# Optimization experiments

Measured on AMD Instinct MI355X. Metric: run time of the kernel, lower is better.

## Reference

```python
import jax, jax.numpy as jnp
import numpy as np

B, T, N, D, E = 16, 12, 512, 128, 32  # batch, time, nodes, model_dim, node_emb_dim


def setup_inputs() -> dict:
    key = jax.random.key(0)
    ks = jax.random.split(key, 7)
    return {
        "value": jax.random.normal(ks[0], (B, T, N, D), dtype=jnp.float32),
        "emb": jax.random.normal(ks[1], (T, N, E), dtype=jnp.float32),
        "attn_mask": jax.random.randint(ks[2], (B, N, N), 0, 2, dtype=jnp.int32),
        "W_qk": jax.random.normal(ks[3], (E, D), dtype=jnp.float32) * (1.0 / np.sqrt(E)),
        "b_qk": jax.random.normal(ks[4], (D,), dtype=jnp.float32) * 0.02,
        "W_v": jax.random.normal(ks[5], (D, D), dtype=jnp.float32) * (1.0 / np.sqrt(D)),
        "b_v": jax.random.normal(ks[6], (D,), dtype=jnp.float32) * 0.02,
    }


def reference(value, emb, attn_mask, W_qk, b_qk, W_v, b_v):
    # qk projection shared between query and key: [T, N, D]
    qk = emb @ W_qk + b_qk
    # query: softmax over feature dim D
    q = jax.nn.softmax(qk, axis=-1)                      # [T, N, D]
    # key: transpose then softmax over node dim N
    k = jax.nn.softmax(jnp.swapaxes(qk, -1, -2), axis=-1)  # [T, D, N]
    # value projection (note: out_proj in __init__ is unused in forward)
    v = value @ W_v + b_v                                # [B, T, N, D]
    # batch-independent base attention score, then broadcast over batch
    score = jnp.einsum('tnd,tdm->tnm', q, k)             # [T, N, N]
    score = jnp.broadcast_to(score[None], (value.shape[0],) + score.shape)  # [B, T, N, N]
    # masked fill: mask [B, N, N] -> [B, 1, N, N]
    score = jnp.where(attn_mask[:, None] == 0, jnp.float32(-1e9), score)
    out = jnp.einsum('btnm,btmd->btnd', score, v)         # [B, T, N, D]
    return out
```

## Files before the change

### kernel.cpp

```cpp
#include <hip/hip_runtime.h>

#define B_ 16
#define T_ 12
#define N_ 512
#define D_ 128
#define E_ 32

typedef __attribute__((ext_vector_type(8))) unsigned short u16x8;
typedef __attribute__((ext_vector_type(8))) __bf16 bf16x8;
typedef __attribute__((ext_vector_type(4))) float f32x4;

static __device__ __forceinline__ unsigned short f2bf(float f) {
    unsigned u = __float_as_uint(f);
    unsigned r = (u + 0x7fffu + ((u >> 16) & 1u)) >> 16;
    return (unsigned short)r;
}

static __device__ __forceinline__ void gld16(const void* src, void* dst) {
    __builtin_amdgcn_global_load_lds(
        (const __attribute__((address_space(1))) unsigned*)src,
        (__attribute__((address_space(3))) unsigned*)dst, 16, 0, 0);
}

__global__ __launch_bounds__(256) void k1(const float* __restrict__ emb,
                                          const float* __restrict__ Wqk,
                                          const float* __restrict__ bqk,
                                          unsigned short* __restrict__ qb,
                                          unsigned short* __restrict__ kN,
                                          const float* __restrict__ Wv,
                                          unsigned short* __restrict__ WvT,
                                          const int* __restrict__ mask,
                                          unsigned* __restrict__ mb) {
    __shared__ __align__(16) char LE[256 * 128];
    __shared__ float red[2][4][8];
    int hwid = blockIdx.x;
    int bid = (hwid & 7) * 144 + (hwid >> 3);
    int tid = threadIdx.x;

    if (bid < 192) {
        int t = bid >> 4;
        int d0 = (bid & 15) * 8;
        int dc = tid & 7, ni = tid >> 3;
        int wave = tid >> 6, lane = tid & 63;
        int l3 = lane >> 3, l7 = lane & 7;
        float wqv[E_];
#pragma unroll
        for (int e = 0; e < E_; ++e) wqv[e] = Wqk[e * D_ + d0 + dc];
        float bq = bqk[d0 + dc];
        const char* eb = (const char*)(emb + (size_t)t * N_ * E_);

        float vals[16];
#pragma unroll
        for (int pass = 0; pass < 2; ++pass) {
#pragma unroll
            for (int it = 0; it < 8; ++it) {
                int rl = it * 32 + wave * 8 + l3;
                int rg = pass * 256 + rl;
                gld16(eb + (size_t)rg * 128 + ((l7 * 16) ^ ((rg & 7) << 4)),
                      LE + (it * 32 + wave * 8) * 128 + lane * 16);
            }
            __syncthreads();
#pragma unroll
            for (int jj = 0; jj < 8; ++jj) {
                int n = pass * 256 + ni + 32 * jj;
                int nl = ni + 32 * jj;
                float a = bq;
#pragma unroll
                for (int s = 0; s < 8; ++s) {
                    f32x4 ev = *(const f32x4*)(LE + nl * 128 +
                                               ((s * 16) ^ ((n & 7) << 4)));
                    a = fmaf(ev[0], wqv[s * 4 + 0], a);
                    a = fmaf(ev[1], wqv[s * 4 + 1], a);
                    a = fmaf(ev[2], wqv[s * 4 + 2], a);
                    a = fmaf(ev[3], wqv[s * 4 + 3], a);
                }
                vals[pass * 8 + jj] = a;
            }
            __syncthreads();
        }

        float mx = -1e30f;
#pragma unroll
        for (int j = 0; j < 16; ++j) mx = fmaxf(mx, vals[j]);
#pragma unroll
        for (int s = 8; s < 64; s <<= 1) mx = fmaxf(mx, __shfl_xor(mx, s));
        int wv = tid >> 6;
        if ((tid & 63) < 8) red[0][wv][dc] = mx;
        __syncthreads();
        mx = fmaxf(fmaxf(red[0][0][dc], red[0][1][dc]),
                   fmaxf(red[0][2][dc], red[0][3][dc]));
        float sum = 0.f;
#pragma unroll
        for (int j = 0; j < 16; ++j) {
            vals[j] = __expf(vals[j] - mx);
            sum += vals[j];
        }
#pragma unroll
        for (int s = 8; s < 64; s <<= 1) sum += __shfl_xor(sum, s);
        if ((tid & 63) < 8) red[1][wv][dc] = sum;
        __syncthreads();
        sum = red[1][0][dc] + red[1][1][dc] + red[1][2][dc] + red[1][3][dc];
        float inv = 1.f / sum;
        unsigned short* op = kN + (size_t)t * N_ * D_ + d0 + dc;
#pragma unroll
        for (int j = 0; j < 16; ++j)
            op[(size_t)(ni + 32 * j) * D_] = f2bf(vals[j] * inv);
        return;
    }

    if (bid < 576) {
        int bid2 = bid - 192;
        int w = tid >> 6, l = tid & 63;
        float wq0[E_], wq1[E_];
#pragma unroll
        for (int e = 0; e < E_; ++e) {
            wq0[e] = Wqk[e * D_ + l];
            wq1[e] = Wqk[e * D_ + l + 64];
        }
        float b0 = bqk[l], b1 = bqk[l + 64];
        for (int rr = 0; rr < 4; ++rr) {
            int tn = bid2 * 16 + w * 4 + rr;
            const float* ep = emb + (size_t)tn * E_;
            float a0 = b0, a1 = b1;
#pragma unroll
            for (int e = 0; e < E_; ++e) {
                float ev = ep[e];
                a0 = fmaf(ev, wq0[e], a0);
                a1 = fmaf(ev, wq1[e], a1);
            }
            float mx = fmaxf(a0, a1);
#pragma unroll
            for (int s = 32; s > 0; s >>= 1) mx = fmaxf(mx, __shfl_xor(mx, s));
            float e0 = __expf(a0 - mx), e1 = __expf(a1 - mx);
            float sum = e0 + e1;
#pragma unroll
            for (int s = 32; s > 0; s >>= 1) sum += __shfl_xor(sum, s);
            float inv = 1.f / sum;
            qb[(size_t)tn * D_ + l] = f2bf(e0 * inv);
            qb[(size_t)tn * D_ + l + 64] = f2bf(e1 * inv);
        }
        return;
    }

    if (bid < 1088) {
        int o = (bid - 576) * 256 + tid;
        const int* mp = mask + (size_t)o * 32;
        unsigned bits = 0;
#pragma unroll
        for (int j = 0; j < 32; j += 4) {
            int4 m4 = *(const int4*)&mp[j];
            bits |= (m4.x ? 1u : 0u) << j;
            bits |= (m4.y ? 1u : 0u) << (j + 1);
            bits |= (m4.z ? 1u : 0u) << (j + 2);
            bits |= (m4.w ? 1u : 0u) << (j + 3);
        }
        mb[o] = bits;
        return;
    }

    {
        int i = (bid - 1088) * 256 + tid;
        int d = i >> 7, k = i & 127;
        WvT[d * 128 + k] = f2bf(Wv[k * 128 + d]);
    }
}

__global__ __launch_bounds__(256, 2) void kF(const unsigned short* __restrict__ qb,
                                             const unsigned short* __restrict__ kN,
                                             unsigned short* __restrict__ sc,
                                             const float* __restrict__ value,
                                             const unsigned short* __restrict__ WvT,
                                             const float* __restrict__ bv,
                                             unsigned short* __restrict__ vT) {
    __shared__ __align__(16) char LA[2][128 * 128];
    __shared__ __align__(16) char LB[2][128 * 128];
    int hwid = blockIdx.x;
    int bid = (hwid & 7) * 120 + (hwid >> 3);
    int tid = threadIdx.x;
    int wave = tid >> 6, lane = tid & 63;
    int q = lane >> 4, lr = lane & 15;
    int rbase = (wave & 1) * 64, cbase = (wave >> 1) * 64;
    int l3 = lane >> 3, l7 = lane & 7;

    f32x4 acc[4][4];
#pragma unroll
    for (int i = 0; i < 4; ++i)
#pragma unroll
        for (int j = 0; j < 4; ++j) acc[i][j] = (f32x4){0.f, 0.f, 0.f, 0.f};

#define STAGE_T(gbase, lb, c)                                                   \
    _Pragma("unroll") for (int it_ = 0; it_ < 4; ++it_) {                       \
        int row_ = it_ * 32 + wave * 8 + l3;                                    \
        gld16((gbase) + (size_t)row_ * 256 + (c) * 128 +                        \
                  ((l7 * 16) ^ ((row_ & 7) << 4)),                              \
              (lb) + (it_ * 32 + wave * 8) * 128 + lane * 16);                  \
    }

#define MFMA_CHUNK(c)                                                           \
    _Pragma("unroll") for (int ksl_ = 0; ksl_ < 2; ++ksl_) {                    \
        bf16x8 a_[4], b_[4];                                                    \
        _Pragma("unroll") for (int i_ = 0; i_ < 4; ++i_) {                      \
            int r_ = rbase + 16 * i_ + lr;                                      \
            a_[i_] = *(const bf16x8*)(LA[c] + r_ * 128 +                        \
                                      ((ksl_ * 64 + q * 16) ^ ((r_ & 7) << 4)));\
        }                                                                       \
        _Pragma("unroll") for (int j_ = 0; j_ < 4; ++j_) {                      \
            int r_ = cbase + 16 * j_ + lr;                                      \
            b_[j_] = *(const bf16x8*)(LB[c] + r_ * 128 +                        \
                                      ((ksl_ * 64 + q * 16) ^ ((r_ & 7) << 4)));\
        }                                                                       \
        _Pragma("unroll") for (int i_ = 0; i_ < 4; ++i_)                        \
            _Pragma("unroll") for (int j_ = 0; j_ < 4; ++j_)                    \
                acc[i_][j_] = __builtin_amdgcn_mfma_f32_16x16x32_bf16(          \
                    a_[i_], b_[j_], acc[i_][j_], 0, 0, 0);                      \
    }

    if (bid < 192) {
        int mt = bid & 3, nt = (bid >> 2) & 3, t = bid >> 4;
        int n0 = nt * 128, m0 = mt * 128;
        const char* qp = (const char*)(qb + (size_t)t * N_ * D_ + (size_t)n0 * D_);
        const char* kp = (const char*)(kN + (size_t)t * N_ * D_ + (size_t)m0 * D_);
        STAGE_T(qp, LA[0], 0)
        STAGE_T(kp, LB[0], 0)
        STAGE_T(qp, LA[1], 1)
        STAGE_T(kp, LB[1], 1)
        asm volatile("s_waitcnt vmcnt(8)" ::: "memory");
        __builtin_amdgcn_sched_barrier(0);
        __builtin_amdgcn_s_barrier();
        __builtin_amdgcn_sched_barrier(0);
        MFMA_CHUNK(0)
        asm volatile("s_waitcnt vmcnt(0)" ::: "memory");
        __builtin_amdgcn_sched_barrier(0);
        __builtin_amdgcn_s_barrier();
        __builtin_amdgcn_sched_barrier(0);
        MFMA_CHUNK(1)

        unsigned short* sp = sc + (size_t)t * N_ * N_;
#pragma unroll
        for (int i = 0; i < 4; ++i)
#pragma unroll
            for (int j = 0; j < 4; ++j) {
                int row0 = n0 + rbase + 16 * i + q * 4;
                int col = m0 + cbase + 16 * j + lr;
#pragma unroll
                for (int e = 0; e < 4; ++e)
                    sp[(size_t)(row0 + e) * N_ + col] = f2bf(acc[i][j][e]);
            }
        return;
    }

    {
        int idx = bid - 192;
        int mt = idx & 3, bt = idx >> 2;
        int m0 = mt * 128;
        const float* vp = value + ((size_t)bt * N_ + m0) * D_;
        const char* wp = (const char*)WvT;
        int g = tid >> 4, c16 = tid & 15;

        float4 v0[8], v1[8];
#pragma unroll
        for (int jj = 0; jj < 8; ++jj)
            v0[jj] = *(const float4*)(vp + (size_t)(g * 8 + jj) * D_ + c16 * 4);
        __builtin_amdgcn_sched_barrier(0);
        STAGE_T(wp, LA[0], 0)
        __builtin_amdgcn_sched_barrier(0);
#pragma unroll
        for (int jj = 0; jj < 8; ++jj)
            v1[jj] = *(const float4*)(vp + (size_t)(g * 8 + jj) * D_ + 64 + c16 * 4);
        __builtin_amdgcn_sched_barrier(0);
        STAGE_T(wp, LA[1], 1)
        __builtin_amdgcn_sched_barrier(0);

#pragma unroll
        for (int jj = 0; jj < 8; ++jj) {
            int row = g * 8 + jj;
            ushort4 o;
            o.x = f2bf(v0[jj].x); o.y = f2bf(v0[jj].y);
            o.z = f2bf(v0[jj].z); o.w = f2bf(v0[jj].w);
            *(ushort4*)(LB[0] + row * 128 + ((c16 * 8) ^ ((row & 7) << 4))) = o;
        }
        asm volatile("s_waitcnt vmcnt(12) lgkmcnt(0)" ::: "memory");
        __builtin_amdgcn_sched_barrier(0);
        __builtin_amdgcn_s_barrier();
        __builtin_amdgcn_sched_barrier(0);
        MFMA_CHUNK(0)
#pragma unroll
        for (int jj = 0; jj < 8; ++jj) {
            int row = g * 8 + jj;
            ushort4 o;
            o.x = f2bf(v1[jj].x); o.y = f2bf(v1[jj].y);
            o.z = f2bf(v1[jj].z); o.w = f2bf(v1[jj].w);
            *(ushort4*)(LB[1] + row * 128 + ((c16 * 8) ^ ((row & 7) << 4))) = o;
        }
        asm volatile("s_waitcnt vmcnt(0) lgkmcnt(0)" ::: "memory");
        __builtin_amdgcn_sched_barrier(0);
        __builtin_amdgcn_s_barrier();
        __builtin_amdgcn_sched_barrier(0);
        MFMA_CHUNK(1)

        unsigned short* op = vT + (size_t)bt * N_ * D_;
#pragma unroll
        for (int i = 0; i < 4; ++i) {
            int row0 = rbase + 16 * i + q * 4;
            float4 bq = *(const float4*)&bv[row0];
#pragma unroll
            for (int j = 0; j < 4; ++j) {
                int col = m0 + cbase + 16 * j + lr;
                op[(size_t)(row0 + 0) * N_ + col] = f2bf(acc[i][j][0] + bq.x);
                op[(size_t)(row0 + 1) * N_ + col] = f2bf(acc[i][j][1] + bq.y);
                op[(size_t)(row0 + 2) * N_ + col] = f2bf(acc[i][j][2] + bq.z);
                op[(size_t)(row0 + 3) * N_ + col] = f2bf(acc[i][j][3] + bq.w);
            }
        }
    }
#undef STAGE_T
#undef MFMA_CHUNK
}

__global__ __launch_bounds__(256, 2) void kC(const unsigned short* __restrict__ sc,
                                             const unsigned* __restrict__ mb,
                                             const unsigned short* __restrict__ vT,
                                             float* __restrict__ out) {
    int hwid = blockIdx.x;
    int w = (hwid & 7) * 96 + (hwid >> 3);
    int n0 = (w & 3) * 128;
    int r = w >> 2;
    int t = r % T_, b = r / T_;
    int tid = threadIdx.x;
    int wave = tid >> 6, lane = tid & 63;
    int q = lane >> 4, lr = lane & 15;
    int rbase = (wave & 1) * 64, cbase = (wave >> 1) * 64;

    __shared__ __align__(16) unsigned short Sb[2][128 * 64];
    __shared__ __align__(16) unsigned short Vb[2][128 * 64];

    const unsigned short* scp = sc + (size_t)t * N_ * N_ + (size_t)n0 * N_;
    const unsigned short* vtp = vT + ((size_t)(b * T_ + t)) * N_ * D_;
    const unsigned* mbp = mb + ((size_t)b * N_ + n0) * 16;
    const unsigned short NEG = 0xCE6E;

    f32x4 acc[4][4];
#pragma unroll
    for (int i = 0; i < 4; ++i)
#pragma unroll
        for (int j = 0; j < 4; ++j) acc[i][j] = (f32x4){0.f, 0.f, 0.f, 0.f};

    int sr = tid >> 1, sh2 = tid & 1;
    const unsigned short* sg = scp + (size_t)sr * N_ + sh2 * 32;
    const unsigned* mwp = mbp + sr * 16 + sh2;
    int swz_r = (sr & 7) << 4;

    int l3 = lane >> 3, l7 = lane & 7;
    int vin = (l7 * 16) ^ (l3 << 4);
    const char* vbase = (const char*)vtp;

    u16x8 sreg[2][4];
    unsigned mwv[2];

#define VISS(buf, kc)                                                           \
    _Pragma("unroll") for (int it_ = 0; it_ < 4; ++it_) {                       \
        int row_ = (it_ * 4 + wave) * 8 + l3;                                   \
        gld16(vbase + (size_t)row_ * 1024 + (kc) * 128 + vin,                   \
              (char*)Vb[buf] + ((it_ * 4 + wave) * 64 + lane) * 16);            \
    }

#define SLOAD(s, kc)                                                            \
    _Pragma("unroll") for (int p_ = 0; p_ < 4; ++p_)                            \
        sreg[s][p_] = *(const u16x8*)(sg + (kc) * 64 + p_ * 8);                 \
    mwv[s] = mwp[(kc) * 2];

#define MERGE(buf, s)                                                           \
    _Pragma("unroll") for (int p_ = 0; p_ < 4; ++p_) {                          \
        unsigned bits_ = mwv[s] >> (p_ * 8);                                    \
        u16x8 o_;                                                               \
        _Pragma("unroll") for (int j_ = 0; j_ < 8; ++j_)                        \
            o_[j_] = ((bits_ >> j_) & 1u) ? sreg[s][p_][j_] : NEG;              \
        *(u16x8*)((char*)Sb[buf] + sr * 128 + ((sh2 * 64 + p_ * 16) ^ swz_r)) = \
            o_;                                                                 \
    }

#define MFMAC(c)                                                                \
    {                                                                           \
        const char* Sbase_ = (const char*)Sb[c];                                \
        const char* Vbase_ = (const char*)Vb[c];                                \
        int swz_l_ = (lr & 7) << 4;                                             \
        _Pragma("unroll") for (int ks_ = 0; ks_ < 2; ++ks_) {                   \
            bf16x8 a_[4], bb_[4];                                               \
            _Pragma("unroll") for (int i_ = 0; i_ < 4; ++i_) {                  \
                int r_ = rbase + 16 * i_ + lr;                                  \
                a_[i_] = *(const bf16x8*)(Sbase_ + r_ * 128 +                   \
                                          ((ks_ * 64 + q * 16) ^ swz_l_));      \
            }                                                                   \
            _Pragma("unroll") for (int j_ = 0; j_ < 4; ++j_) {                  \
                int d_ = cbase + 16 * j_ + lr;                                  \
                bb_[j_] = *(const bf16x8*)(Vbase_ + d_ * 128 +                  \
                                           ((ks_ * 64 + q * 16) ^ swz_l_));     \
            }                                                                   \
            _Pragma("unroll") for (int i_ = 0; i_ < 4; ++i_)                    \
                _Pragma("unroll") for (int j_ = 0; j_ < 4; ++j_)                \
                    acc[i_][j_] = __builtin_amdgcn_mfma_f32_16x16x32_bf16(      \
                        a_[i_], bb_[j_], acc[i_][j_], 0, 0, 0);                 \
        }                                                                       \
    }

    VISS(0, 0)
    SLOAD(0, 0)
    SLOAD(1, 1)
    asm volatile("s_waitcnt vmcnt(5)" ::: "memory");
    __builtin_amdgcn_sched_barrier(0);
    MERGE(0, 0)
    asm volatile("s_waitcnt lgkmcnt(0)" ::: "memory");
    __builtin_amdgcn_s_barrier();
    __builtin_amdgcn_sched_barrier(0);

#pragma unroll
    for (int kc = 0; kc < 8; ++kc) {
        int cur = kc & 1, nxt = cur ^ 1;
        if (kc < 7) { VISS(nxt, kc + 1) }
        if (kc < 6) { SLOAD(cur, kc + 2) }
        if (kc < 6) {
            asm volatile("s_waitcnt vmcnt(9)" ::: "memory");
        } else if (kc == 6) {
            asm volatile("s_waitcnt vmcnt(4)" ::: "memory");
        } else {
            asm volatile("s_waitcnt vmcnt(0)" ::: "memory");
        }
        __builtin_amdgcn_sched_barrier(0);
        MFMAC(cur)
        if (kc < 7) { MERGE(nxt, nxt) }
        asm volatile("s_waitcnt lgkmcnt(0)" ::: "memory");
        if (kc < 7) {
            __builtin_amdgcn_s_barrier();
            __builtin_amdgcn_sched_barrier(0);
        }
    }

#undef VISS
#undef SLOAD
#undef MERGE
#undef MFMAC

    float* ob = out + ((size_t)(b * T_ + t)) * N_ * D_;
#pragma unroll
    for (int i = 0; i < 4; ++i) {
#pragma unroll
        for (int j = 0; j < 4; ++j) {
            int row0 = n0 + rbase + 16 * i + q * 4;
            int col = cbase + 16 * j + lr;
#pragma unroll
            for (int e = 0; e < 4; ++e)
                ob[(size_t)(row0 + e) * D_ + col] = acc[i][j][e];
        }
    }
}

extern "C" void kernel_launch(void* const* d_in, const int* in_sizes, int n_in,
                              void* d_out, int out_size, void* d_ws, size_t ws_size,
                              hipStream_t stream) {
    const float* value = (const float*)d_in[0];
    const float* emb   = (const float*)d_in[1];
    const int*   mask  = (const int*)d_in[2];
    const float* Wqk   = (const float*)d_in[3];
    const float* bqk   = (const float*)d_in[4];
    const float* Wv    = (const float*)d_in[5];
    const float* bvv   = (const float*)d_in[6];
    float* out = (float*)d_out;

    float* ws = (float*)d_ws;
    unsigned short* qb   = (unsigned short*)(ws + 786432);
    unsigned short* kNb  = (unsigned short*)(ws + 1179648);
    unsigned short* scb  = (unsigned short*)(ws + 1572864);
    unsigned short* vtb  = (unsigned short*)(ws + 3145728);
    unsigned short* WvTb = (unsigned short*)(ws + 9437184);
    unsigned*       mbp  = (unsigned*)(ws + 9445376);

    k1<<<1152, 256, 0, stream>>>(emb, Wqk, bqk, qb, kNb, Wv, WvTb, mask, mbp);
    kF<<<960, 256, 0, stream>>>(qb, kNb, scb, value, WvTb, bvv, vtb);
    kC<<<768, 256, 0, stream>>>(scb, mbp, vtb, out);
}
```

Before: 159.7 us.

## Move mask bit-packing into kF and single-buffer score tile in kC for occupancy

The mask-to-bitmask packing blocks move from the first kernel into the kF launch as extra trailing blocks, so they run alongside the score/value GEMM blocks instead of lengthening k1. In kC the score LDS tile is single-buffered with precomputed write pointers, and launch bounds rise to 3 blocks per CU. The pipeline is simplified: the next chunk is prefetched, the current one is merged into LDS, and the MFMA is bracketed by two barriers. This cuts LDS use so more blocks fit per CU, at the cost of an extra barrier per step and less global-load lookahead.

```diff
diff --git a/kernel.cpp b/kernel.cpp
--- a/kernel.cpp
+++ b/kernel.cpp
@@ -28,13 +28,11 @@
                                           unsigned short* __restrict__ qb,
                                           unsigned short* __restrict__ kN,
                                           const float* __restrict__ Wv,
-                                          unsigned short* __restrict__ WvT,
-                                          const int* __restrict__ mask,
-                                          unsigned* __restrict__ mb) {
+                                          unsigned short* __restrict__ WvT) {
     __shared__ __align__(16) char LE[256 * 128];
     __shared__ float red[2][4][8];
     int hwid = blockIdx.x;
-    int bid = (hwid & 7) * 144 + (hwid >> 3);
+    int bid = (hwid & 7) * 80 + (hwid >> 3);
     int tid = threadIdx.x;
 
     if (bid < 192) {
@@ -142,8 +140,30 @@
         return;
     }
 
-    if (bid < 1088) {
-        int o = (bid - 576) * 256 + tid;
+    {
+        int i = (bid - 576) * 256 + tid;
+        int d = i >> 7, k = i & 127;
+        WvT[d * 128 + k] = f2bf(Wv[k * 128 + d]);
+    }
+}
+
+__global__ __launch_bounds__(256, 2) void kF(const unsigned short* __restrict__ qb,
+                                             const unsigned short* __restrict__ kN,
+                                             unsigned short* __restrict__ sc,
+                                             const float* __restrict__ value,
+                                             const unsigned short* __restrict__ WvT,
+                                             const float* __restrict__ bv,
+                                             unsigned short* __restrict__ vT,
+                                             const int* __restrict__ mask,
+                                             unsigned* __restrict__ mb) {
+    __shared__ __align__(16) char LA[2][128 * 128];
+    __shared__ __align__(16) char LB[2][128 * 128];
+    int hwid = blockIdx.x;
+    int bid = (hwid & 7) * 184 + (hwid >> 3);
+    int tid = threadIdx.x;
+
+    if (bid >= 960) {
+        int o = (bid - 960) * 256 + tid;
         const int* mp = mask + (size_t)o * 32;
         unsigned bits = 0;
 #pragma unroll
@@ -158,25 +178,6 @@
         return;
     }
 
-    {
-        int i = (bid - 1088) * 256 + tid;
-        int d = i >> 7, k = i & 127;
-        WvT[d * 128 + k] = f2bf(Wv[k * 128 + d]);
-    }
-}
-
-__global__ __launch_bounds__(256, 2) void kF(const unsigned short* __restrict__ qb,
-                                             const unsigned short* __restrict__ kN,
-                                             unsigned short* __restrict__ sc,
-                                             const float* __restrict__ value,
-                                             const unsigned short* __restrict__ WvT,
-                                             const float* __restrict__ bv,
-                                             unsigned short* __restrict__ vT) {
-    __shared__ __align__(16) char LA[2][128 * 128];
-    __shared__ __align__(16) char LB[2][128 * 128];
-    int hwid = blockIdx.x;
-    int bid = (hwid & 7) * 120 + (hwid >> 3);
-    int tid = threadIdx.x;
     int wave = tid >> 6, lane = tid & 63;
     int q = lane >> 4, lr = lane & 15;
     int rbase = (wave & 1) * 64, cbase = (wave >> 1) * 64;
@@ -317,7 +318,7 @@
 #undef MFMA_CHUNK
 }
 
-__global__ __launch_bounds__(256, 2) void kC(const unsigned short* __restrict__ sc,
+__global__ __launch_bounds__(256, 3) void kC(const unsigned short* __restrict__ sc,
                                              const unsigned* __restrict__ mb,
                                              const unsigned short* __restrict__ vT,
                                              float* __restrict__ out) {
@@ -331,8 +332,8 @@
     int q = lane >> 4, lr = lane & 15;
     int rbase = (wave & 1) * 64, cbase = (wave >> 1) * 64;
 
-    __shared__ __align__(16) unsigned short Sb[2][128 * 64];
-    __shared__ __align__(16) unsigned short Vb[2][128 * 64];
+    __shared__ unsigned short Sb[128 * 64];
+    __shared__ unsigned short Vb[2][128 * 64];
 
     const unsigned short* scp = sc + (size_t)t * N_ * N_ + (size_t)n0 * N_;
     const unsigned short* vtp = vT + ((size_t)(b * T_ + t)) * N_ * D_;
@@ -349,6 +350,10 @@
     const unsigned short* sg = scp + (size_t)sr * N_ + sh2 * 32;
     const unsigned* mwp = mbp + sr * 16 + sh2;
     int swz_r = (sr & 7) << 4;
+    char* Sw[4];
+#pragma unroll
+    for (int p = 0; p < 4; ++p)
+        Sw[p] = (char*)Sb + sr * 128 + ((sh2 * 64 + p * 16) ^ swz_r);
 
     int l3 = lane >> 3, l7 = lane & 7;
     int vin = (l7 * 16) ^ (l3 << 4);
@@ -369,19 +374,18 @@
         sreg[s][p_] = *(const u16x8*)(sg + (kc) * 64 + p_ * 8);                 \
     mwv[s] = mwp[(kc) * 2];
 
-#define MERGE(buf, s)                                                           \
+#define MERGE(s)                                                                \
     _Pragma("unroll") for (int p_ = 0; p_ < 4; ++p_) {                          \
         unsigned bits_ = mwv[s] >> (p_ * 8);                                    \
         u16x8 o_;                                                               \
         _Pragma("unroll") for (int j_ = 0; j_ < 8; ++j_)                        \
             o_[j_] = ((bits_ >> j_) & 1u) ? sreg[s][p_][j_] : NEG;              \
-        *(u16x8*)((char*)Sb[buf] + sr * 128 + ((sh2 * 64 + p_ * 16) ^ swz_r)) = \
-            o_;                                                                 \
+        *(u16x8*)Sw[p_] = o_;                                                   \
     }
 
 #define MFMAC(c)                                                                \
     {                                                                           \
-        const char* Sbase_ = (const char*)Sb[c];                                \
+        const char* Sbase_ = (const char*)Sb;                                   \
         const char* Vbase_ = (const char*)Vb[c];                                \
         int swz_l_ = (lr & 7) << 4;                                             \
         _Pragma("unroll") for (int ks_ = 0; ks_ < 2; ++ks_) {                   \
@@ -405,34 +409,22 @@
 
     VISS(0, 0)
     SLOAD(0, 0)
-    SLOAD(1, 1)
-    asm volatile("s_waitcnt vmcnt(5)" ::: "memory");
-    __builtin_amdgcn_sched_barrier(0);
-    MERGE(0, 0)
-    asm volatile("s_waitcnt lgkmcnt(0)" ::: "memory");
-    __builtin_amdgcn_s_barrier();
-    __builtin_amdgcn_sched_barrier(0);
 
 #pragma unroll
     for (int kc = 0; kc < 8; ++kc) {
-        int cur = kc & 1, nxt = cur ^ 1;
-        if (kc < 7) { VISS(nxt, kc + 1) }
-        if (kc < 6) { SLOAD(cur, kc + 2) }
-        if (kc < 6) {
-            asm volatile("s_waitcnt vmcnt(9)" ::: "memory");
-        } else if (kc == 6) {
-            asm volatile("s_waitcnt vmcnt(4)" ::: "memory");
-        } else {
-            asm volatile("s_waitcnt vmcnt(0)" ::: "memory");
-        }
+        const int cur = kc & 1, nxt = cur ^ 1;
+        if (kc < 7) {
+            VISS(nxt, kc + 1)
+            SLOAD(nxt, kc + 1)
+        }
+        __builtin_amdgcn_sched_barrier(0);
+        MERGE(cur)
+        asm volatile("s_waitcnt lgkmcnt(0)" ::: "memory");
+        __builtin_amdgcn_s_barrier();
         __builtin_amdgcn_sched_barrier(0);
         MFMAC(cur)
-        if (kc < 7) { MERGE(nxt, nxt) }
-        asm volatile("s_waitcnt lgkmcnt(0)" ::: "memory");
-        if (kc < 7) {
-            __builtin_amdgcn_s_barrier();
-            __builtin_amdgcn_sched_barrier(0);
-        }
+        __builtin_amdgcn_s_barrier();
+        __builtin_amdgcn_sched_barrier(0);
     }
 
 #undef VISS
@@ -474,7 +466,7 @@
     unsigned short* WvTb = (unsigned short*)(ws + 9437184);
     unsigned*       mbp  = (unsigned*)(ws + 9445376);
 
-    k1<<<1152, 256, 0, stream>>>(emb, Wqk, bqk, qb, kNb, Wv, WvTb, mask, mbp);
-    kF<<<960, 256, 0, stream>>>(qb, kNb, scb, value, WvTb, bvv, vtb);
+    k1<<<640, 256, 0, stream>>>(emb, Wqk, bqk, qb, kNb, Wv, WvTb);
+    kF<<<1472, 256, 0, stream>>>(qb, kNb, scb, value, WvTb, bvv, vtb, mask, mbp);
     kC<<<768, 256, 0, stream>>>(scb, mbp, vtb, out);
 }
```

New measurement: 160.8 us. No clear change (+0.7%).
